# Kernel optimization log

Measured on AMD Instinct MI355X. Metric: run time of the kernel, lower is better.

## Reference

```python
import jax, jax.numpy as jnp
import numpy as np

N, M, DIST, HEADS, D, C, DFFN = 16384, 16, 2, 8, 256, 64, 512
DH = D // HEADS
GRID = 128
BLOCK = 2048  # mirrors torch batch_size loop in find_neighboring_voxels_optimized
EPS = 1e-5


def _neighbors(coords_f, src, m, dist):
    """Blockwise Manhattan-distance topk neighbor gather.
    coords_f: (N,3) float voxel coords; src: (N,D) features.
    Returns (N, m, D) neighbor features, zero-filled where fewer than m in range."""
    n = coords_f.shape[0]
    qblocks = coords_f.reshape(-1, BLOCK, 3)

    def one_block(cb):
        # (BLOCK, N) Manhattan distances
        d = jnp.abs(cb[:, None, :] - coords_f[None, :, :]).sum(-1)
        d = jnp.where(d <= dist, d, jnp.inf)
        vals, idx = jax.lax.top_k(-d, m)          # nearest m (self first: dist 0)
        valid = (vals > -jnp.inf)[..., None]
        return jnp.where(valid, src[idx], jnp.zeros((), src.dtype))

    return jax.lax.map(one_block, qblocks).reshape(n, m, src.shape[-1])


def _layernorm(x, g, b):
    mu = x.mean(-1, keepdims=True)
    var = ((x - mu) ** 2).mean(-1, keepdims=True)
    return (x - mu) * jax.lax.rsqrt(var + EPS) * g + b


def setup_inputs() -> dict:
    key = jax.random.key(0)
    ks = jax.random.split(key, 32)
    p = lambda i, shape, s: jax.random.normal(ks[i], shape, dtype=jnp.float32) * s
    z = lambda shape: jnp.zeros(shape, dtype=jnp.float32)
    o = lambda shape: jnp.ones(shape, dtype=jnp.float32)
    return {
        "coords": jax.random.randint(ks[0], (N, 3), 0, GRID, dtype=jnp.int32),
        "features": jax.random.normal(ks[1], (N, C), dtype=jnp.float32),
        "pe_w1": p(2, (3, D // 2), 0.5), "pe_b1": z((D // 2,)),
        "pe_w2": p(3, (D // 2, D), 0.08), "pe_b2": z((D,)),
        "proj_w": p(4, (C, D), 0.12), "proj_b": z((D,)),
        "wq": p(5, (D, D), 0.06), "bq": z((D,)),
        "wk": p(6, (D, D), 0.06), "bk": z((D,)),
        "wv": p(7, (D, D), 0.06), "bv": z((D,)),
        "wo": p(8, (D, D), 0.06), "bo": z((D,)),
        "ffn_w1": p(9, (D, DFFN), 0.06), "ffn_b1": z((DFFN,)),
        "ffn_w2": p(10, (DFFN, D), 0.04), "ffn_b2": z((D,)),
        "ln_g": o((D,)), "ln_b": z((D,)),
        "fus_w1": p(11, (D, C), 0.06), "fus_b1": z((C,)),
        "fus_w2": p(12, (2 * C, C), 0.09), "fus_b2": z((C,)),
        "bn_g": o((C,)), "bn_b": z((C,)),
    }


def reference(coords, features, pe_w1, pe_b1, pe_w2, pe_b2, proj_w, proj_b,
              wq, bq, wk, bk, wv, bv, wo, bo,
              ffn_w1, ffn_b1, ffn_w2, ffn_b2, ln_g, ln_b,
              fus_w1, fus_b1, fus_w2, fus_b2, bn_g, bn_b):
    coords_f = coords.astype(jnp.float32)
    # dynamic learnable positional encoding on normalized coords
    xn = coords_f / (GRID - 1)
    pe = jax.nn.relu(xn @ pe_w1 + pe_b1) @ pe_w2 + pe_b2
    src = features @ proj_w + proj_b + pe                       # (N, D)

    nf = _neighbors(coords_f, src, M, DIST)                     # (N, M, D)
    query = nf[:, 0, :]                                         # (N, D) self-feature

    # multihead attention: query len 1, key len M, batch N
    q = (query @ wq + bq).reshape(N, HEADS, DH)
    k = (nf @ wk + bk).reshape(N, M, HEADS, DH)
    v = (nf @ wv + bv).reshape(N, M, HEADS, DH)
    scores = jnp.einsum('nhd,nmhd->nhm', q, k) / jnp.sqrt(jnp.float32(DH))
    attn = jax.nn.softmax(scores, axis=-1)
    ao = jnp.einsum('nhm,nmhd->nhd', attn, v).reshape(N, D) @ wo + bo  # (N, D)

    # FFN with residual + LayerNorm (dropout=0 / eval)
    h = jax.nn.relu(ao @ ffn_w1 + ffn_b1) @ ffn_w2 + ffn_b2
    y = _layernorm(ao + h, ln_g, ln_b)                          # (N, D)

    # EnhancedFusion: project, concat, linear, BatchNorm1d (batch stats), ReLU
    t = y @ fus_w1 + fus_b1                                     # (N, C)
    f = jnp.concatenate([features, t], axis=1) @ fus_w2 + fus_b2
    mu = f.mean(0)
    var = ((f - mu) ** 2).mean(0)
    f = (f - mu) * jax.lax.rsqrt(var + EPS) * bn_g + bn_b
    return jax.nn.relu(f)                                       # (N, C)
```

## Files before the change

### kernel.cpp

```cpp
#include <hip/hip_runtime.h>
#include <stdint.h>

typedef unsigned short u16;
typedef unsigned int   u32;
typedef __attribute__((ext_vector_type(8))) short short8;
typedef __attribute__((ext_vector_type(4))) float f32x4;

static constexpr int kN = 16384;
static constexpr float kEPS = 1e-5f;

__device__ __forceinline__ u16 f2bf(float x) {
  u32 u = __float_as_uint(x);
  u32 r = (u + 0x7fffu + ((u >> 16) & 1u)) >> 16;
  return (u16)r;
}
__device__ __forceinline__ float bf2f(u16 x) {
  return __uint_as_float(((u32)x) << 16);
}
__device__ __forceinline__ void ldbf8(const u16* p, float* o) {
  uint4 v = *(const uint4*)p;
  o[0] = __uint_as_float(v.x << 16);  o[1] = __uint_as_float(v.x & 0xffff0000u);
  o[2] = __uint_as_float(v.y << 16);  o[3] = __uint_as_float(v.y & 0xffff0000u);
  o[4] = __uint_as_float(v.z << 16);  o[5] = __uint_as_float(v.z & 0xffff0000u);
  o[6] = __uint_as_float(v.w << 16);  o[7] = __uint_as_float(v.w & 0xffff0000u);
}


__global__ __launch_bounds__(256) void k_hist(const int* __restrict__ coords,
                                              u32* __restrict__ cnt) {
  int n = blockIdx.x * 256 + threadIdx.x;
  int c = coords[n * 3] * 128 + coords[n * 3 + 1];
  atomicAdd(&cnt[c], 1u);
}

__global__ __launch_bounds__(256) void k_scan(const u32* __restrict__ cnt,
                                              u32* __restrict__ startb) {
  __shared__ u32 tots[256];
  int t = threadIdx.x;
  int base = t * 64;
  u32 s = 0;
  for (int i = 0; i < 64; i++) s += cnt[base + i];
  tots[t] = s;
  __syncthreads();
  if (t == 0) {
    u32 run = 0;
    for (int i = 0; i < 256; i++) { u32 v = tots[i]; tots[i] = run; run += v; }
  }
  __syncthreads();
  u32 run = tots[t];
  for (int i = 0; i < 64; i++) { startb[base + i] = run; run += cnt[base + i]; }
}

__global__ __launch_bounds__(256) void k_scatter(const int* __restrict__ coords,
                                                 const u32* __restrict__ startb,
                                                 u32* __restrict__ cursor,
                                                 u32* __restrict__ pts) {
  int n = blockIdx.x * 256 + threadIdx.x;
  int x = coords[n * 3], y = coords[n * 3 + 1], z = coords[n * 3 + 2];
  int c = x * 128 + y;
  u32 slot = atomicAdd(&cursor[c], 1u);
  pts[startb[c] + slot] = ((u32)z << 14) | (u32)n;
}

__global__ __launch_bounds__(256) void k_select(const int* __restrict__ coords,
                                                const u32* __restrict__ startb,
                                                const u32* __restrict__ cnt,
                                                const u32* __restrict__ pts,
                                                int* __restrict__ idxo) {
  int n = blockIdx.x * 256 + threadIdx.x;
  int x = coords[n * 3], y = coords[n * 3 + 1], z = coords[n * 3 + 2];
  u32 best[16];
#pragma unroll
  for (int j = 0; j < 16; j++) best[j] = 0xFFFFFFFFu;
  const int dxs[13] = {0, -1, 1, 0, 0, -2, 2, 0, 0, -1, -1, 1, 1};
  const int dys[13] = {0, 0, 0, -1, 1, 0, 0, -2, 2, -1, 1, -1, 1};
  const int dbs[13] = {0, 1, 1, 1, 1, 2, 2, 2, 2, 2, 2, 2, 2};
#pragma unroll
  for (int t = 0; t < 13; t++) {
    int xx = x + dxs[t], yy = y + dys[t];
    if (xx < 0 || xx > 127 || yy < 0 || yy > 127) continue;
    int c = xx * 128 + yy;
    u32 s0 = startb[c], e0 = s0 + cnt[c];
    for (u32 i = s0; i < e0; ++i) {
      u32 p = pts[i];
      int zq = (int)(p >> 14);
      int id = (int)(p & 16383u);
      int az = z - zq; az = az < 0 ? -az : az;
      int dd = dbs[t] + az;
      u32 key = (dd <= 2) ? (((u32)dd << 14) | (u32)id) : 0xFFFFFFFFu;
#pragma unroll
      for (int j = 0; j < 16; j++) {
        u32 lo = min(best[j], key);
        u32 hi = max(best[j], key);
        best[j] = lo; key = hi;
      }
    }
  }
#pragma unroll
  for (int j = 0; j < 16; j++)
    idxo[n * 16 + j] = (best[j] == 0xFFFFFFFFu) ? -1 : (int)(best[j] & 16383u);
}

struct WSet {
  const float* s[8]; u16* d[8];
  int K[8]; int N[8]; int dstride[8]; int coff[8];
};

__global__ __launch_bounds__(256) void k_setup(WSet ws,
                                               u32* __restrict__ zero_area,
                                               const float* __restrict__ proj_b,
                                               const float* __restrict__ pe_b2,
                                               float* __restrict__ pbc,
                                               const float* __restrict__ uw1,
                                               const float* __restrict__ ub1,
                                               const float* __restrict__ uw2,
                                               const float* __restrict__ ub2,
                                               u16* __restrict__ W2f,
                                               float* __restrict__ bbf) {
  int w = blockIdx.y;
  if (w == 8) {
    zero_area[blockIdx.x * 256 + threadIdx.x] = 0u;
    return;
  }
  if (w == 9) {
    int bx = blockIdx.x;
    if (bx == 0) {
      pbc[threadIdx.x] = proj_b[threadIdx.x] + pe_b2[threadIdx.x];
    } else if (bx < 65) {
      int n = bx - 1;
      int k = threadIdx.x;
      float s = 0.f;
      for (int j = 0; j < 64; j++) s += uw1[k * 64 + j] * uw2[(64 + j) * 64 + n];
      W2f[n * 320 + k] = f2bf(s);
      if (k < 64) W2f[n * 320 + 256 + k] = f2bf(uw2[k * 64 + n]);
      if (k == 0) {
        float b = ub2[n];
        for (int j = 0; j < 64; j++) b += ub1[j] * uw2[(64 + j) * 64 + n];
        bbf[n] = b;
      }
    }
    return;
  }
  const float* S = ws.s[w]; u16* D = ws.d[w];
  int K = ws.K[w], N = ws.N[w], ds = ws.dstride[w], co = ws.coff[w];
  int ntx = N >> 5, tiles = ntx * (K >> 5);
  int t = blockIdx.x;
  if (t >= tiles) return;
  int n0 = (t % ntx) * 32, k0 = (t / ntx) * 32;
  __shared__ float st[32][33];
  int tr = threadIdx.x >> 3, tc4 = (threadIdx.x & 7) * 4;
  float4 v = *(const float4*)(S + (size_t)(k0 + tr) * N + n0 + tc4);
  st[tc4 + 0][tr] = v.x; st[tc4 + 1][tr] = v.y;
  st[tc4 + 2][tr] = v.z; st[tc4 + 3][tr] = v.w;
  __syncthreads();
  u16 o4[4];
  o4[0] = f2bf(st[tr][tc4 + 0]); o4[1] = f2bf(st[tr][tc4 + 1]);
  o4[2] = f2bf(st[tr][tc4 + 2]); o4[3] = f2bf(st[tr][tc4 + 3]);
  *(uint2*)(D + (size_t)(n0 + tr) * ds + co + k0 + tc4) = *(uint2*)o4;
}

__global__ __launch_bounds__(256) void k_prep(const int* __restrict__ coords,
                                              const float* __restrict__ feats,
                                              const float* __restrict__ pw1,
                                              const float* __restrict__ pb1,
                                              u16* __restrict__ A1,
                                              u16* __restrict__ A2) {
  int r0 = blockIdx.x * 32;
#pragma unroll
  for (int s = 0; s < 3; s++) {
    int j = threadIdx.x + s * 256;
    int row = j / 24, seg = j % 24;
    int n = r0 + row;
    u16 o[8];
    if (seg < 8) {
      const float* fp = feats + (size_t)n * 64 + seg * 8;
      float4 a = *(const float4*)fp;
      float4 b = *(const float4*)(fp + 4);
      o[0] = f2bf(a.x); o[1] = f2bf(a.y); o[2] = f2bf(a.z); o[3] = f2bf(a.w);
      o[4] = f2bf(b.x); o[5] = f2bf(b.y); o[6] = f2bf(b.z); o[7] = f2bf(b.w);
      *(uint4*)(A2 + (size_t)n * 320 + 256 + seg * 8) = *(uint4*)o;
    } else {
      int jj0 = (seg - 8) * 8;
      float x0 = (float)coords[n * 3 + 0] * (1.f / 127.f);
      float x1 = (float)coords[n * 3 + 1] * (1.f / 127.f);
      float x2 = (float)coords[n * 3 + 2] * (1.f / 127.f);
#pragma unroll
      for (int u = 0; u < 8; u++) {
        int jj = jj0 + u;
        float hv = pb1[jj] + x0 * pw1[jj] + x1 * pw1[128 + jj] + x2 * pw1[256 + jj];
        o[u] = f2bf(fmaxf(hv, 0.f));
      }
    }
    *(uint4*)(A1 + (size_t)n * 192 + seg * 8) = *(uint4*)o;
  }
}

template <int BM, int BN, int ACT, int OUTBF, int ADD>
__global__ __launch_bounds__(256) void k_mfma_gemm(
    const u16* __restrict__ A, const u16* __restrict__ WT,
    const float* __restrict__ bias,
    void* __restrict__ Cout,
    const u16* __restrict__ Addp,
    int M, int K, int N) {
  constexpr int GA = BM / 64;
  constexpr int GT = (BM + BN) / 64;
  constexpr int AI = BM / 32;
  constexpr int BI = BN / 32;
  __shared__ __align__(16) u16 As[BM * 32];
  __shared__ __align__(16) u16 Bs[BN * 32];
  const int tid = threadIdx.x;
  const int wave = tid >> 6, lane = tid & 63;
  const int bm = blockIdx.y * BM, bn = blockIdx.x * BN;
  const int wr = (wave >> 1) * (BM / 2), wc = (wave & 1) * (BN / 2);

  f32x4 acc[AI][BI];
#pragma unroll
  for (int i = 0; i < AI; i++)
#pragma unroll
    for (int j = 0; j < BI; j++)
#pragma unroll
      for (int r = 0; r < 4; r++) acc[i][j][r] = 0.f;

  for (int k0 = 0; k0 < K; k0 += 32) {
#pragma unroll
    for (int i = 0; i < GT; i++) {
      int g = i * 256 + wave * 64 + lane;
      if (i < GA) {
        int row = g >> 2, ko = (g & 3) * 8;
        __builtin_amdgcn_global_load_lds(
            (const __attribute__((address_space(1))) void*)(A + (size_t)(bm + row) * K + k0 + ko),
            (__attribute__((address_space(3))) void*)(As + (size_t)g * 8), 16, 0, 0);
      } else {
        int g2 = g - GA * 256;
        int row = g2 >> 2, ko = (g2 & 3) * 8;
        __builtin_amdgcn_global_load_lds(
            (const __attribute__((address_space(1))) void*)(WT + (size_t)(bn + row) * K + k0 + ko),
            (__attribute__((address_space(3))) void*)(Bs + (size_t)g2 * 8), 16, 0, 0);
      }
    }
    __syncthreads();
    short8 af[AI], bg[BI];
#pragma unroll
    for (int i = 0; i < AI; i++)
      af[i] = *(const short8*)&As[(wr + i * 16 + (lane & 15)) * 32 + (lane >> 4) * 8];
#pragma unroll
    for (int j = 0; j < BI; j++)
      bg[j] = *(const short8*)&Bs[(wc + j * 16 + (lane & 15)) * 32 + (lane >> 4) * 8];
#pragma unroll
    for (int i = 0; i < AI; i++)
#pragma unroll
      for (int j = 0; j < BI; j++)
        acc[i][j] = __builtin_amdgcn_mfma_f32_16x16x32_bf16(af[i], bg[j], acc[i][j], 0, 0, 0);
    __syncthreads();
  }

#pragma unroll
  for (int j = 0; j < BI; j++) {
    int cc = bn + wc + j * 16 + (lane & 15);
    float bval = bias ? bias[cc] : 0.f;
#pragma unroll
    for (int i = 0; i < AI; i++) {
      int rbase = bm + wr + i * 16 + (lane >> 4) * 4;
#pragma unroll
      for (int r = 0; r < 4; r++) {
        float v = acc[i][j][r] + bval;
        size_t o = (size_t)(rbase + r) * N + cc;
        if (ADD) v += bf2f(Addp[o]);
        if (ACT) v = fmaxf(v, 0.f);
        if (OUTBF) ((u16*)Cout)[o] = f2bf(v);
        else       ((float*)Cout)[o] = v;
      }
    }
  }
}

__global__ __launch_bounds__(256) void k_attn(const u16* __restrict__ QKV,
                                              const u32* __restrict__ pts,
                                              const int* __restrict__ idx,
                                              const float* __restrict__ bq,
                                              const float* __restrict__ bk,
                                              const float* __restrict__ bv,
                                              u16* __restrict__ outp) {
  int gid = blockIdx.x * 256 + threadIdx.x;
  int n = (int)(pts[gid >> 3] & 16383u), h = gid & 7;
  const int* ip = idx + n * 16;
  const int hb = h * 32;
  float q[32];
  {
    int i0 = ip[0];
    const u16* qp = QKV + (size_t)i0 * 768 + hb;
#pragma unroll
    for (int j = 0; j < 32; j += 8) ldbf8(qp + j, &q[j]);
#pragma unroll
    for (int j = 0; j < 32; j++) q[j] += bq[hb + j];
  }
// ... 26 lines not shown
#pragma unroll
  for (int j = 0; j < 32; j++) o[j] = 0.f;
#pragma unroll
  for (int m = 0; m < 16; m++) {
    if (ii[m] >= 0) {
      const u16* vp = QKV + (size_t)ii[m] * 768 + 512 + hb;
      float vv[32];
#pragma unroll
      for (int j = 0; j < 32; j += 8) ldbf8(vp + j, &vv[j]);
#pragma unroll
      for (int j = 0; j < 32; j++) o[j] += s[m] * vv[j];
    }
  }
  u16* op = outp + (size_t)n * 256 + hb;
#pragma unroll
  for (int j = 0; j < 32; j += 8) {
    u16 tmp[8];
#pragma unroll
    for (int jj = 0; jj < 8; jj++) tmp[jj] = f2bf(o[j + jj] * inv + bv[hb + j + jj]);
    *(uint4*)(op + j) = *(uint4*)tmp;
  }
}

__global__ __launch_bounds__(256) void k_ln(const u16* __restrict__ xx,
                                            const float* __restrict__ g,
                                            const float* __restrict__ b,
                                            u16* __restrict__ A2) {
  int row = blockIdx.x * 4 + (threadIdx.x >> 6);
  int lane = threadIdx.x & 63;
  uint2 raw = *(const uint2*)(xx + (size_t)row * 256 + lane * 4);
  float x0 = __uint_as_float(raw.x << 16), x1 = __uint_as_float(raw.x & 0xffff0000u);
  float x2 = __uint_as_float(raw.y << 16), x3 = __uint_as_float(raw.y & 0xffff0000u);
  float sm = x0 + x1 + x2 + x3;
#pragma unroll
  for (int off = 1; off < 64; off <<= 1) sm += __shfl_xor(sm, off);
  float mu = sm * (1.f / 256.f);
  float d0 = x0 - mu, d1 = x1 - mu, d2 = x2 - mu, d3 = x3 - mu;
  float sq = d0 * d0 + d1 * d1 + d2 * d2 + d3 * d3;
#pragma unroll
  for (int off = 1; off < 64; off <<= 1) sq += __shfl_xor(sq, off);
  float rstd = rsqrtf(sq * (1.f / 256.f) + kEPS);
  float4 gv = *(const float4*)(g + lane * 4);
  float4 bv4 = *(const float4*)(b + lane * 4);
  u16 o[4];
  o[0] = f2bf(d0 * rstd * gv.x + bv4.x); o[1] = f2bf(d1 * rstd * gv.y + bv4.y);
  o[2] = f2bf(d2 * rstd * gv.z + bv4.z); o[3] = f2bf(d3 * rstd * gv.w + bv4.w);
  *(uint2*)(A2 + (size_t)row * 320 + lane * 4) = *(uint2*)o;
}

__global__ __launch_bounds__(256) void k_stats(const float* __restrict__ f,
                                               float* __restrict__ pS, float* __restrict__ pQ) {
  int col = threadIdx.x & 63, rc = threadIdx.x >> 6;
  int r0 = blockIdx.x * 128 + rc * 32;
  float s = 0.f, q = 0.f;
  for (int r = 0; r < 32; r++) {
    float v = f[(size_t)(r0 + r) * 64 + col];
    s += v; q += v * v;
  }
  __shared__ float ls[4][64], lq[4][64];
  ls[rc][col] = s; lq[rc][col] = q;
  __syncthreads();
  if (rc == 0) {
    s = ls[0][col] + ls[1][col] + ls[2][col] + ls[3][col];
    q = lq[0][col] + lq[1][col] + lq[2][col] + lq[3][col];
    pS[blockIdx.x * 64 + col] = s;
    pQ[blockIdx.x * 64 + col] = q;
  }
}

__global__ __launch_bounds__(64) void k_bnfin(const float* __restrict__ pS,
                                              const float* __restrict__ pQ,
                                              const float* __restrict__ g,
                                              const float* __restrict__ b,
                                              float* __restrict__ coef,
                                              float* __restrict__ shift) {
  int c = threadIdx.x;
  float s = 0.f, q = 0.f;
  for (int i = 0; i < 128; i++) { s += pS[i * 64 + c]; q += pQ[i * 64 + c]; }
  float mu = s * (1.f / 16384.f);
  float var = q * (1.f / 16384.f) - mu * mu;
  float cf = rsqrtf(var + kEPS) * g[c];
  coef[c] = cf;
  shift[c] = b[c] - mu * cf;
}

__global__ __launch_bounds__(256) void k_bnapply(const float* __restrict__ f,
                                                 const float* __restrict__ coef,
                                                 const float* __restrict__ shift,
                                                 float* __restrict__ out) {
  int gid = blockIdx.x * 256 + threadIdx.x;
  int e = gid * 4, col = e & 63;
  float4 v = *(const float4*)(f + e);
  float4 cf = *(const float4*)(coef + col);
  float4 sh = *(const float4*)(shift + col);
  float4 o;
  o.x = fmaxf(v.x * cf.x + sh.x, 0.f);
  o.y = fmaxf(v.y * cf.y + sh.y, 0.f);
  o.z = fmaxf(v.z * cf.z + sh.z, 0.f);
  o.w = fmaxf(v.w * cf.w + sh.w, 0.f);
  *(float4*)(out + e) = o;
}

extern "C" void kernel_launch(void* const* d_in, const int* in_sizes, int n_in,
                              void* d_out, int out_size, void* d_ws, size_t ws_size,
                              hipStream_t stream) {
  (void)in_sizes; (void)n_in; (void)out_size; (void)ws_size;
// ... 10 lines not shown
  const float* wk  = (const float*)d_in[10];
  const float* bk  = (const float*)d_in[11];
  const float* wv  = (const float*)d_in[12];
  const float* bv  = (const float*)d_in[13];
  const float* wo  = (const float*)d_in[14];
  const float* bo  = (const float*)d_in[15];
  const float* fw1 = (const float*)d_in[16];
  const float* fb1 = (const float*)d_in[17];
  const float* fw2 = (const float*)d_in[18];
  const float* fb2 = (const float*)d_in[19];
  const float* lng = (const float*)d_in[20];
  const float* lnb = (const float*)d_in[21];
  const float* uw1 = (const float*)d_in[22];
  const float* ub1 = (const float*)d_in[23];
  const float* uw2 = (const float*)d_in[24];
  const float* ub2 = (const float*)d_in[25];
  const float* bng = (const float*)d_in[26];
  const float* bnb = (const float*)d_in[27];
  float* out = (float*)d_out;

  char* Wc = (char*)d_ws;
  const size_t MB = 1u << 20;
  u16*   A1    = (u16*)(Wc + 0 * MB);
  u16*   srcb  = (u16*)(Wc + 6 * MB);
  u16*   QKVb  = (u16*)(Wc + 14 * MB);
  u16*   aoInB = (u16*)(Wc + 38 * MB);
  u16*   aoB   = (u16*)(Wc + 46 * MB);
  u16*   h1B   = (u16*)(Wc + 54 * MB);
  u16*   xBb   = (u16*)(Wc + 70 * MB);
  u16*   A2    = (u16*)(Wc + 78 * MB);
  float* fB    = (float*)(Wc + 0 * MB);

  u16* qkvT  = (u16*)(Wc + 96 * MB);
  u16* woT   = qkvT + 196608;
  u16* fw1T  = woT + 65536;
  u16* fw2T  = fw1T + 131072;
  u16* W1T   = fw2T + 131072;
  u16* W2f   = W1T + 49152;
  float* pbc = (float*)(W2f + 20480);
  float* bbf = pbc + 256;

  u32* cnt    = (u32*)(Wc + 98 * MB);
  u32* cursor = cnt + 16384;
  u32* startb = cnt + 32768;
  u32* pts    = cnt + 49152;
  int* idxb   = (int*)(cnt + 65536);
  float* pS    = (float*)(cnt + 65536 + 262144);
  float* pQ    = pS + 8192;
  float* coefb = pQ + 8192;
  float* shb   = coefb + 64;

  WSet ws;
  ws.s[0] = wq;     ws.d[0] = qkvT;          ws.K[0] = 256; ws.N[0] = 256; ws.dstride[0] = 256; ws.coff[0] = 0;
  ws.s[1] = wk;     ws.d[1] = qkvT + 65536;  ws.K[1] = 256; ws.N[1] = 256; ws.dstride[1] = 256; ws.coff[1] = 0;
  ws.s[2] = wv;     ws.d[2] = qkvT + 131072; ws.K[2] = 256; ws.N[2] = 256; ws.dstride[2] = 256; ws.coff[2] = 0;
  ws.s[3] = wo;     ws.d[3] = woT;           ws.K[3] = 256; ws.N[3] = 256; ws.dstride[3] = 256; ws.coff[3] = 0;
  ws.s[4] = fw1;    ws.d[4] = fw1T;          ws.K[4] = 256; ws.N[4] = 512; ws.dstride[4] = 256; ws.coff[4] = 0;
  ws.s[5] = fw2;    ws.d[5] = fw2T;          ws.K[5] = 512; ws.N[5] = 256; ws.dstride[5] = 512; ws.coff[5] = 0;
  ws.s[6] = proj_w; ws.d[6] = W1T;           ws.K[6] = 64;  ws.N[6] = 256; ws.dstride[6] = 192; ws.coff[6] = 0;
  ws.s[7] = pe_w2;  ws.d[7] = W1T;           ws.K[7] = 128; ws.N[7] = 256; ws.dstride[7] = 192; ws.coff[7] = 64;
  k_setup<<<dim3(128, 10), 256, 0, stream>>>(ws, cnt, proj_b, pe_b2, pbc,
                                             uw1, ub1, uw2, ub2, W2f, bbf);

  k_hist<<<64, 256, 0, stream>>>(coords, cnt);
  k_scan<<<1, 256, 0, stream>>>(cnt, startb);
  k_scatter<<<64, 256, 0, stream>>>(coords, startb, cursor, pts);
  k_select<<<64, 256, 0, stream>>>(coords, startb, cnt, pts, idxb);

  k_prep<<<512, 256, 0, stream>>>(coords, feats, pe_w1, pe_b1, A1, A2);

  k_mfma_gemm<64, 64, 0, 1, 0><<<dim3(4, 256), 256, 0, stream>>>(A1, W1T, pbc, srcb, nullptr, kN, 192, 256);
  k_mfma_gemm<64, 64, 0, 1, 0><<<dim3(12, 256), 256, 0, stream>>>(srcb, qkvT, nullptr, QKVb, nullptr, kN, 256, 768);

  k_attn<<<512, 256, 0, stream>>>(QKVb, pts, idxb, bq, bk, bv, aoInB);

  k_mfma_gemm<64, 64, 0, 1, 0><<<dim3(4, 256), 256, 0, stream>>>(aoInB, woT, bo, aoB, nullptr, kN, 256, 256);
  k_mfma_gemm<64, 64, 1, 1, 0><<<dim3(8, 256), 256, 0, stream>>>(aoB, fw1T, fb1, h1B, nullptr, kN, 256, 512);
  k_mfma_gemm<64, 64, 0, 1, 1><<<dim3(4, 256), 256, 0, stream>>>(h1B, fw2T, fb2, xBb, aoB, kN, 512, 256);

  k_ln<<<4096, 256, 0, stream>>>(xBb, lng, lnb, A2);

  k_mfma_gemm<64, 64, 0, 0, 0><<<dim3(1, 256), 256, 0, stream>>>(A2, W2f, bbf, fB, nullptr, kN, 320, 64);

  k_stats<<<128, 256, 0, stream>>>(fB, pS, pQ);
  k_bnfin<<<1, 64, 0, stream>>>(pS, pQ, bng, bnb, coefb, shb);
  k_bnapply<<<1024, 256, 0, stream>>>(fB, coefb, shb, out);
}
```

Baseline: 257.6 us.

## Fuse pipeline into few kernels with grid barriers and on-chip intermediates

```diff
diff --git a/kernel.cpp b/kernel.cpp
--- a/kernel.cpp
+++ b/kernel.cpp
@@ -24,81 +24,10 @@
   o[4] = __uint_as_float(v.z << 16);  o[5] = __uint_as_float(v.z & 0xffff0000u);
   o[6] = __uint_as_float(v.w << 16);  o[7] = __uint_as_float(v.w & 0xffff0000u);
 }
-
-
-__global__ __launch_bounds__(256) void k_hist(const int* __restrict__ coords,
-                                              u32* __restrict__ cnt) {
-  int n = blockIdx.x * 256 + threadIdx.x;
-  int c = coords[n * 3] * 128 + coords[n * 3 + 1];
-  atomicAdd(&cnt[c], 1u);
-}
-
-__global__ __launch_bounds__(256) void k_scan(const u32* __restrict__ cnt,
-                                              u32* __restrict__ startb) {
-  __shared__ u32 tots[256];
-  int t = threadIdx.x;
-  int base = t * 64;
-  u32 s = 0;
-  for (int i = 0; i < 64; i++) s += cnt[base + i];
-  tots[t] = s;
-  __syncthreads();
-  if (t == 0) {
-    u32 run = 0;
-    for (int i = 0; i < 256; i++) { u32 v = tots[i]; tots[i] = run; run += v; }
-  }
-  __syncthreads();
-  u32 run = tots[t];
-  for (int i = 0; i < 64; i++) { startb[base + i] = run; run += cnt[base + i]; }
-}
-
-__global__ __launch_bounds__(256) void k_scatter(const int* __restrict__ coords,
-                                                 const u32* __restrict__ startb,
-                                                 u32* __restrict__ cursor,
-                                                 u32* __restrict__ pts) {
-  int n = blockIdx.x * 256 + threadIdx.x;
-  int x = coords[n * 3], y = coords[n * 3 + 1], z = coords[n * 3 + 2];
-  int c = x * 128 + y;
-  u32 slot = atomicAdd(&cursor[c], 1u);
-  pts[startb[c] + slot] = ((u32)z << 14) | (u32)n;
-}
-
-__global__ __launch_bounds__(256) void k_select(const int* __restrict__ coords,
-                                                const u32* __restrict__ startb,
-                                                const u32* __restrict__ cnt,
-                                                const u32* __restrict__ pts,
-                                                int* __restrict__ idxo) {
-  int n = blockIdx.x * 256 + threadIdx.x;
-  int x = coords[n * 3], y = coords[n * 3 + 1], z = coords[n * 3 + 2];
-  u32 best[16];
-#pragma unroll
-  for (int j = 0; j < 16; j++) best[j] = 0xFFFFFFFFu;
-  const int dxs[13] = {0, -1, 1, 0, 0, -2, 2, 0, 0, -1, -1, 1, 1};
-  const int dys[13] = {0, 0, 0, -1, 1, 0, 0, -2, 2, -1, 1, -1, 1};
-  const int dbs[13] = {0, 1, 1, 1, 1, 2, 2, 2, 2, 2, 2, 2, 2};
-#pragma unroll
-  for (int t = 0; t < 13; t++) {
-    int xx = x + dxs[t], yy = y + dys[t];
-    if (xx < 0 || xx > 127 || yy < 0 || yy > 127) continue;
-    int c = xx * 128 + yy;
-    u32 s0 = startb[c], e0 = s0 + cnt[c];
-    for (u32 i = s0; i < e0; ++i) {
-      u32 p = pts[i];
-      int zq = (int)(p >> 14);
-      int id = (int)(p & 16383u);
-      int az = z - zq; az = az < 0 ? -az : az;
-      int dd = dbs[t] + az;
-      u32 key = (dd <= 2) ? (((u32)dd << 14) | (u32)id) : 0xFFFFFFFFu;
-#pragma unroll
-      for (int j = 0; j < 16; j++) {
-        u32 lo = min(best[j], key);
-        u32 hi = max(best[j], key);
-        best[j] = lo; key = hi;
-      }
-    }
-  }
-#pragma unroll
-  for (int j = 0; j < 16; j++)
-    idxo[n * 16 + j] = (best[j] == 0xFFFFFFFFu) ? -1 : (int)(best[j] & 16383u);
+__device__ __forceinline__ void gll16(const u16* g, u16* l) {
+  __builtin_amdgcn_global_load_lds(
+      (const __attribute__((address_space(1))) void*)g,
+      (__attribute__((address_space(3))) void*)l, 16, 0, 0);
 }
 
 struct WSet {
@@ -116,10 +45,17 @@
                                                const float* __restrict__ uw2,
                                                const float* __restrict__ ub2,
                                                u16* __restrict__ W2f,
-                                               float* __restrict__ bbf) {
+                                               float* __restrict__ bbf,
+                                               const int* __restrict__ coords,
+                                               const float* __restrict__ feats,
+                                               const float* __restrict__ pw1,
+                                               const float* __restrict__ pb1,
+                                               u16* __restrict__ A1,
+                                               u16* __restrict__ A2) {
   int w = blockIdx.y;
   if (w == 8) {
-    zero_area[blockIdx.x * 256 + threadIdx.x] = 0u;
+    int idx = blockIdx.x * 256 + threadIdx.x;
+    if (idx < 32960) zero_area[idx] = 0u;
     return;
   }
   if (w == 9) {
@@ -141,6 +77,39 @@
     }
     return;
   }
+  if (w == 10) {
+    int r0 = blockIdx.x * 32;
+#pragma unroll
+    for (int s = 0; s < 3; s++) {
+      int j = threadIdx.x + s * 256;
+      int row = j / 24, seg = j % 24;
+      int n = r0 + row;
+      u16 o[8];
+      if (seg < 8) {
+        const float* fp = feats + (size_t)n * 64 + seg * 8;
+        float4 a = *(const float4*)fp;
+        float4 b = *(const float4*)(fp + 4);
+        o[0] = f2bf(a.x); o[1] = f2bf(a.y); o[2] = f2bf(a.z); o[3] = f2bf(a.w);
+        o[4] = f2bf(b.x); o[5] = f2bf(b.y); o[6] = f2bf(b.z); o[7] = f2bf(b.w);
+        *(uint4*)(A2 + (size_t)n * 320 + 256 + seg * 8) = *(uint4*)o;
+      } else {
+        int jj0 = (seg - 8) * 8;
+        float x0 = (float)coords[n * 3 + 0] * (1.f / 127.f);
+        float x1 = (float)coords[n * 3 + 1] * (1.f / 127.f);
+        float x2 = (float)coords[n * 3 + 2] * (1.f / 127.f);
+#pragma unroll
+        for (int u = 0; u < 8; u++) {
+          int jj = jj0 + u;
+          float hv = pb1[jj] + x0 * pw1[jj] + x1 * pw1[128 + jj] + x2 * pw1[256 + jj];
+          o[u] = f2bf(fmaxf(hv, 0.f));
+        }
+        *(uint4*)(A1 + (size_t)n * 192 + seg * 8) = *(uint4*)o;
+        continue;
+      }
+      *(uint4*)(A1 + (size_t)n * 192 + seg * 8) = *(uint4*)o;
+    }
+    return;
+  }
   const float* S = ws.s[w]; u16* D = ws.d[w];
   int K = ws.K[w], N = ws.N[w], ds = ws.dstride[w], co = ws.coff[w];
   int ntx = N >> 5, tiles = ntx * (K >> 5);
@@ -159,118 +128,195 @@
   *(uint2*)(D + (size_t)(n0 + tr) * ds + co + k0 + tc4) = *(uint2*)o4;
 }
 
-__global__ __launch_bounds__(256) void k_prep(const int* __restrict__ coords,
-                                              const float* __restrict__ feats,
-                                              const float* __restrict__ pw1,
-                                              const float* __restrict__ pb1,
-                                              u16* __restrict__ A1,
-                                              u16* __restrict__ A2) {
-  int r0 = blockIdx.x * 32;
-#pragma unroll
-  for (int s = 0; s < 3; s++) {
-    int j = threadIdx.x + s * 256;
-    int row = j / 24, seg = j % 24;
-    int n = r0 + row;
-    u16 o[8];
-    if (seg < 8) {
-      const float* fp = feats + (size_t)n * 64 + seg * 8;
-      float4 a = *(const float4*)fp;
-      float4 b = *(const float4*)(fp + 4);
-      o[0] = f2bf(a.x); o[1] = f2bf(a.y); o[2] = f2bf(a.z); o[3] = f2bf(a.w);
-      o[4] = f2bf(b.x); o[5] = f2bf(b.y); o[6] = f2bf(b.z); o[7] = f2bf(b.w);
-      *(uint4*)(A2 + (size_t)n * 320 + 256 + seg * 8) = *(uint4*)o;
-    } else {
-      int jj0 = (seg - 8) * 8;
-      float x0 = (float)coords[n * 3 + 0] * (1.f / 127.f);
-      float x1 = (float)coords[n * 3 + 1] * (1.f / 127.f);
-      float x2 = (float)coords[n * 3 + 2] * (1.f / 127.f);
-#pragma unroll
-      for (int u = 0; u < 8; u++) {
-        int jj = jj0 + u;
-        float hv = pb1[jj] + x0 * pw1[jj] + x1 * pw1[128 + jj] + x2 * pw1[256 + jj];
-        o[u] = f2bf(fmaxf(hv, 0.f));
-      }
-    }
-    *(uint4*)(A1 + (size_t)n * 192 + seg * 8) = *(uint4*)o;
-  }
-}
-
-template <int BM, int BN, int ACT, int OUTBF, int ADD>
-__global__ __launch_bounds__(256) void k_mfma_gemm(
-    const u16* __restrict__ A, const u16* __restrict__ WT,
-    const float* __restrict__ bias,
-    void* __restrict__ Cout,
-    const u16* __restrict__ Addp,
-    int M, int K, int N) {
-  constexpr int GA = BM / 64;
-  constexpr int GT = (BM + BN) / 64;
-  constexpr int AI = BM / 32;
-  constexpr int BI = BN / 32;
-  __shared__ __align__(16) u16 As[BM * 32];
-  __shared__ __align__(16) u16 Bs[BN * 32];
+__device__ __forceinline__ void gbar(u32* bar, u32 target) {
+  __syncthreads();
+  if (threadIdx.x == 0) {
+    __threadfence();
+    __hip_atomic_fetch_add(bar, 1u, __ATOMIC_RELEASE, __HIP_MEMORY_SCOPE_AGENT);
+    while (__hip_atomic_load(bar, __ATOMIC_ACQUIRE, __HIP_MEMORY_SCOPE_AGENT) < target) {}
+    __threadfence();
+  }
+  __syncthreads();
+}
+
+__global__ __launch_bounds__(256) void k_grid(const int* __restrict__ coords,
+                                              u32* __restrict__ cnt,
+                                              u32* __restrict__ cursor,
+                                              u32* __restrict__ startb,
+                                              u32* __restrict__ pts,
+                                              int* __restrict__ idxo,
+                                              u32* __restrict__ bar) {
+  int n = blockIdx.x * 256 + threadIdx.x;
+  int x = coords[n * 3], y = coords[n * 3 + 1], z = coords[n * 3 + 2];
+  int c = x * 128 + y;
+  atomicAdd(&cnt[c], 1u);
+  gbar(bar, 64);
+  if (blockIdx.x == 0) {
+    __shared__ u32 tots[256];
+    int t = threadIdx.x;
+    int base = t * 64;
+    u32 s = 0;
+    for (int i = 0; i < 64; i++) s += cnt[base + i];
+    tots[t] = s;
+    __syncthreads();
+    if (t == 0) {
+      u32 run = 0;
+      for (int i = 0; i < 256; i++) { u32 v = tots[i]; tots[i] = run; run += v; }
+    }
+    __syncthreads();
+    u32 run = tots[t];
+    for (int i = 0; i < 64; i++) { startb[base + i] = run; run += cnt[base + i]; }
+  }
+  gbar(bar, 128);
+  {
+    u32 slot = atomicAdd(&cursor[c], 1u);
+    pts[startb[c] + slot] = ((u32)z << 14) | (u32)n;
+  }
+  gbar(bar, 192);
+  {
+    u32 best[16];
+#pragma unroll
+    for (int j = 0; j < 16; j++) best[j] = 0xFFFFFFFFu;
+    const int dxs[13] = {0, -1, 1, 0, 0, -2, 2, 0, 0, -1, -1, 1, 1};
+    const int dys[13] = {0, 0, 0, -1, 1, 0, 0, -2, 2, -1, 1, -1, 1};
+    const int dbs[13] = {0, 1, 1, 1, 1, 2, 2, 2, 2, 2, 2, 2, 2};
+#pragma unroll
+    for (int t = 0; t < 13; t++) {
+      int xx = x + dxs[t], yy = y + dys[t];
+      if (xx < 0 || xx > 127 || yy < 0 || yy > 127) continue;
+      int cc = xx * 128 + yy;
+      u32 s0 = startb[cc], e0 = s0 + cnt[cc];
+      for (u32 i = s0; i < e0; ++i) {
+        u32 p = pts[i];
+        int zq = (int)(p >> 14);
+        int id = (int)(p & 16383u);
+        int az = z - zq; az = az < 0 ? -az : az;
+        int dd = dbs[t] + az;
+        u32 key = (dd <= 2) ? (((u32)dd << 14) | (u32)id) : 0xFFFFFFFFu;
+#pragma unroll
+        for (int j = 0; j < 16; j++) {
+          u32 lo = min(best[j], key);
+          u32 hi = max(best[j], key);
+          best[j] = lo; key = hi;
+        }
+      }
+    }
+#pragma unroll
+    for (int j = 0; j < 16; j++)
+      idxo[n * 16 + j] = (best[j] == 0xFFFFFFFFu) ? -1 : (int)(best[j] & 16383u);
+  }
+}
+
+__global__ __launch_bounds__(256) void k_src_qkv(const u16* __restrict__ A1,
+                                                 const u16* __restrict__ W1T,
+                                                 const float* __restrict__ pbc,
+                                                 const u16* __restrict__ qkvT,
+                                                 u16* __restrict__ QKV) {
+  __shared__ __align__(16) u16 reg1[16896];
+  __shared__ __align__(16) u16 srcL[16896];
+  __shared__ __align__(16) u16 Bs[2048];
   const int tid = threadIdx.x;
   const int wave = tid >> 6, lane = tid & 63;
-  const int bm = blockIdx.y * BM, bn = blockIdx.x * BN;
-  const int wr = (wave >> 1) * (BM / 2), wc = (wave & 1) * (BN / 2);
-
-  f32x4 acc[AI][BI];
-#pragma unroll
-  for (int i = 0; i < AI; i++)
-#pragma unroll
-    for (int j = 0; j < BI; j++)
-#pragma unroll
-      for (int r = 0; r < 4; r++) acc[i][j][r] = 0.f;
-
-  for (int k0 = 0; k0 < K; k0 += 32) {
-#pragma unroll
-    for (int i = 0; i < GT; i++) {
-      int g = i * 256 + wave * 64 + lane;
-      if (i < GA) {
+  const int bm = blockIdx.x * 64;
+  const int wr = (wave >> 1) * 32, wc = (wave & 1) * 32;
+  const int fr = lane & 15, fk = (lane >> 4) * 8, rq = (lane >> 4) * 4;
+
+#pragma unroll
+  for (int s = 0; s < 6; s++) {
+    int c = tid + s * 256;
+    int row = c / 24, kc = c % 24;
+    *(uint4*)&reg1[row * 200 + kc * 8] =
+        *(const uint4*)(A1 + (size_t)(bm + row) * 192 + kc * 8);
+  }
+  __syncthreads();
+
+  for (int nc = 0; nc < 4; nc++) {
+    f32x4 acc[2][2];
+#pragma unroll
+    for (int i = 0; i < 2; i++)
+#pragma unroll
+      for (int j = 0; j < 2; j++)
+#pragma unroll
+        for (int r = 0; r < 4; r++) acc[i][j][r] = 0.f;
+    for (int k0 = 0; k0 < 192; k0 += 32) {
+      {
+        int g = wave * 64 + lane;
         int row = g >> 2, ko = (g & 3) * 8;
-        __builtin_amdgcn_global_load_lds(
-            (const __attribute__((address_space(1))) void*)(A + (size_t)(bm + row) * K + k0 + ko),
-            (__attribute__((address_space(3))) void*)(As + (size_t)g * 8), 16, 0, 0);
-      } else {
-        int g2 = g - GA * 256;
-        int row = g2 >> 2, ko = (g2 & 3) * 8;
-        __builtin_amdgcn_global_load_lds(
-            (const __attribute__((address_space(1))) void*)(WT + (size_t)(bn + row) * K + k0 + ko),
-            (__attribute__((address_space(3))) void*)(Bs + (size_t)g2 * 8), 16, 0, 0);
-      }
+        gll16(W1T + (size_t)(nc * 64 + row) * 192 + k0 + ko, Bs + g * 8);
+      }
+      __syncthreads();
+      short8 af[2], bg[2];
+#pragma unroll
+      for (int i = 0; i < 2; i++)
+        af[i] = *(const short8*)&reg1[(wr + i * 16 + fr) * 200 + k0 + fk];
+#pragma unroll
+      for (int j = 0; j < 2; j++)
+        bg[j] = *(const short8*)&Bs[(wc + j * 16 + fr) * 32 + fk];
+#pragma unroll
+      for (int i = 0; i < 2; i++)
+#pragma unroll
+        for (int j = 0; j < 2; j++)
+          acc[i][j] = __builtin_amdgcn_mfma_f32_16x16x32_bf16(af[i], bg[j], acc[i][j], 0, 0, 0);
+      __syncthreads();
+    }
+#pragma unroll
+    for (int j = 0; j < 2; j++) {
+      int col = nc * 64 + wc + j * 16 + fr;
+      float bv = pbc[col];
+#pragma unroll
+      for (int i = 0; i < 2; i++) {
+        int rb = wr + i * 16 + rq;
+#pragma unroll
+        for (int r = 0; r < 4; r++)
+          srcL[(rb + r) * 264 + col] = f2bf(acc[i][j][r] + bv);
+      }
+    }
+  }
+  __syncthreads();
+
+  for (int qc = 0; qc < 12; qc++) {
+#pragma unroll
+    for (int s = 0; s < 8; s++) {
+      int c = tid + s * 256;
+      int row = c >> 5, kc = c & 31;
+      *(uint4*)&reg1[row * 264 + kc * 8] =
+          *(const uint4*)(qkvT + (size_t)(qc * 64 + row) * 256 + kc * 8);
     }
     __syncthreads();
-    short8 af[AI], bg[BI];
-#pragma unroll
-    for (int i = 0; i < AI; i++)
-      af[i] = *(const short8*)&As[(wr + i * 16 + (lane & 15)) * 32 + (lane >> 4) * 8];
-#pragma unroll
-    for (int j = 0; j < BI; j++)
-      bg[j] = *(const short8*)&Bs[(wc + j * 16 + (lane & 15)) * 32 + (lane >> 4) * 8];
-#pragma unroll
-    for (int i = 0; i < AI; i++)
-#pragma unroll
-      for (int j = 0; j < BI; j++)
-        acc[i][j] = __builtin_amdgcn_mfma_f32_16x16x32_bf16(af[i], bg[j], acc[i][j], 0, 0, 0);
+    f32x4 acc[2][2];
+#pragma unroll
+    for (int i = 0; i < 2; i++)
+#pragma unroll
+      for (int j = 0; j < 2; j++)
+#pragma unroll
+        for (int r = 0; r < 4; r++) acc[i][j][r] = 0.f;
+#pragma unroll
+    for (int k0 = 0; k0 < 256; k0 += 32) {
+      short8 af[2], bg[2];
+#pragma unroll
+      for (int i = 0; i < 2; i++)
+        af[i] = *(const short8*)&srcL[(wr + i * 16 + fr) * 264 + k0 + fk];
+#pragma unroll
+      for (int j = 0; j < 2; j++)
+        bg[j] = *(const short8*)&reg1[(wc + j * 16 + fr) * 264 + k0 + fk];
+#pragma unroll
+      for (int i = 0; i < 2; i++)
+#pragma unroll
+        for (int j = 0; j < 2; j++)
+          acc[i][j] = __builtin_amdgcn_mfma_f32_16x16x32_bf16(af[i], bg[j], acc[i][j], 0, 0, 0);
+    }
+#pragma unroll
+    for (int j = 0; j < 2; j++) {
+      int col = qc * 64 + wc + j * 16 + fr;
+#pragma unroll
+      for (int i = 0; i < 2; i++) {
+        int rb = wr + i * 16 + rq;
+#pragma unroll
+        for (int r = 0; r < 4; r++)
+          QKV[(size_t)(bm + rb + r) * 768 + col] = f2bf(acc[i][j][r]);
+      }
+    }
     __syncthreads();
-  }
-
-#pragma unroll
-  for (int j = 0; j < BI; j++) {
-    int cc = bn + wc + j * 16 + (lane & 15);
-    float bval = bias ? bias[cc] : 0.f;
-#pragma unroll
-    for (int i = 0; i < AI; i++) {
-      int rbase = bm + wr + i * 16 + (lane >> 4) * 4;
-#pragma unroll
-      for (int r = 0; r < 4; r++) {
-        float v = acc[i][j][r] + bval;
-        size_t o = (size_t)(rbase + r) * N + cc;
-        if (ADD) v += bf2f(Addp[o]);
-        if (ACT) v = fmaxf(v, 0.f);
-        if (OUTBF) ((u16*)Cout)[o] = f2bf(v);
-        else       ((float*)Cout)[o] = v;
-      }
-    }
   }
 }
 
@@ -343,66 +389,315 @@
   }
 }
 
-__global__ __launch_bounds__(256) void k_ln(const u16* __restrict__ xx,
-                                            const float* __restrict__ g,
-                                            const float* __restrict__ b,
-                                            u16* __restrict__ A2) {
-  int row = blockIdx.x * 4 + (threadIdx.x >> 6);
-  int lane = threadIdx.x & 63;
-  uint2 raw = *(const uint2*)(xx + (size_t)row * 256 + lane * 4);
-  float x0 = __uint_as_float(raw.x << 16), x1 = __uint_as_float(raw.x & 0xffff0000u);
-  float x2 = __uint_as_float(raw.y << 16), x3 = __uint_as_float(raw.y & 0xffff0000u);
-  float sm = x0 + x1 + x2 + x3;
-#pragma unroll
-  for (int off = 1; off < 64; off <<= 1) sm += __shfl_xor(sm, off);
-  float mu = sm * (1.f / 256.f);
-  float d0 = x0 - mu, d1 = x1 - mu, d2 = x2 - mu, d3 = x3 - mu;
-  float sq = d0 * d0 + d1 * d1 + d2 * d2 + d3 * d3;
-#pragma unroll
-  for (int off = 1; off < 64; off <<= 1) sq += __shfl_xor(sq, off);
-  float rstd = rsqrtf(sq * (1.f / 256.f) + kEPS);
-  float4 gv = *(const float4*)(g + lane * 4);
-  float4 bv4 = *(const float4*)(b + lane * 4);
-  u16 o[4];
-  o[0] = f2bf(d0 * rstd * gv.x + bv4.x); o[1] = f2bf(d1 * rstd * gv.y + bv4.y);
-  o[2] = f2bf(d2 * rstd * gv.z + bv4.z); o[3] = f2bf(d3 * rstd * gv.w + bv4.w);
-  *(uint2*)(A2 + (size_t)row * 320 + lane * 4) = *(uint2*)o;
-}
-
-__global__ __launch_bounds__(256) void k_stats(const float* __restrict__ f,
-                                               float* __restrict__ pS, float* __restrict__ pQ) {
-  int col = threadIdx.x & 63, rc = threadIdx.x >> 6;
-  int r0 = blockIdx.x * 128 + rc * 32;
-  float s = 0.f, q = 0.f;
-  for (int r = 0; r < 32; r++) {
-    float v = f[(size_t)(r0 + r) * 64 + col];
-    s += v; q += v * v;
-  }
-  __shared__ float ls[4][64], lq[4][64];
-  ls[rc][col] = s; lq[rc][col] = q;
-  __syncthreads();
-  if (rc == 0) {
-    s = ls[0][col] + ls[1][col] + ls[2][col] + ls[3][col];
-    q = lq[0][col] + lq[1][col] + lq[2][col] + lq[3][col];
-    pS[blockIdx.x * 64 + col] = s;
-    pQ[blockIdx.x * 64 + col] = q;
-  }
-}
-
-__global__ __launch_bounds__(64) void k_bnfin(const float* __restrict__ pS,
-                                              const float* __restrict__ pQ,
-                                              const float* __restrict__ g,
-                                              const float* __restrict__ b,
+__global__ __launch_bounds__(256) void k_ffn_ln(const u16* __restrict__ aoIn,
+                                                const u16* __restrict__ woT,
+                                                const float* __restrict__ bo,
+                                                const u16* __restrict__ fw1T,
+                                                const float* __restrict__ fb1,
+                                                const u16* __restrict__ fw2T,
+                                                const float* __restrict__ fb2,
+                                                const float* __restrict__ lng,
+                                                const float* __restrict__ lnb,
+                                                u16* __restrict__ A2) {
+  __shared__ __align__(16) u16 aoL[16896];
+  __shared__ __align__(16) u16 h1L[16896];
+  __shared__ __align__(16) u16 As[2048];
+  __shared__ __align__(16) u16 Bs[2048];
+  const int tid = threadIdx.x;
+  const int wave = tid >> 6, lane = tid & 63;
+  const int bm = blockIdx.x * 64;
+  const int wr = (wave >> 1) * 32, wc = (wave & 1) * 32;
+  const int fr = lane & 15, fk = (lane >> 4) * 8, rq = (lane >> 4) * 4;
+  const int g = wave * 64 + lane;
+  const int grow = g >> 2, gko = (g & 3) * 8;
+
+  for (int nc = 0; nc < 4; nc++) {
+    f32x4 acc[2][2];
+#pragma unroll
+    for (int i = 0; i < 2; i++)
+#pragma unroll
+      for (int j = 0; j < 2; j++)
+#pragma unroll
+        for (int r = 0; r < 4; r++) acc[i][j][r] = 0.f;
+    for (int k0 = 0; k0 < 256; k0 += 32) {
+      gll16(aoIn + (size_t)(bm + grow) * 256 + k0 + gko, As + g * 8);
+      gll16(woT + (size_t)(nc * 64 + grow) * 256 + k0 + gko, Bs + g * 8);
+      __syncthreads();
+      short8 af[2], bg[2];
+#pragma unroll
+      for (int i = 0; i < 2; i++)
+        af[i] = *(const short8*)&As[(wr + i * 16 + fr) * 32 + fk];
+#pragma unroll
+      for (int j = 0; j < 2; j++)
+        bg[j] = *(const short8*)&Bs[(wc + j * 16 + fr) * 32 + fk];
+#pragma unroll
+      for (int i = 0; i < 2; i++)
+#pragma unroll
+        for (int j = 0; j < 2; j++)
+          acc[i][j] = __builtin_amdgcn_mfma_f32_16x16x32_bf16(af[i], bg[j], acc[i][j], 0, 0, 0);
+      __syncthreads();
+    }
+#pragma unroll
+    for (int j = 0; j < 2; j++) {
+      int col = nc * 64 + wc + j * 16 + fr;
+      float bv = bo[col];
+#pragma unroll
+      for (int i = 0; i < 2; i++) {
+        int rb = wr + i * 16 + rq;
+#pragma unroll
+        for (int r = 0; r < 4; r++)
+          aoL[(rb + r) * 264 + col] = f2bf(acc[i][j][r] + bv);
+      }
+    }
+  }
+  __syncthreads();
+
+  f32x4 xacc[4][2][2];
+#pragma unroll
+  for (int xc = 0; xc < 4; xc++)
+#pragma unroll
+    for (int i = 0; i < 2; i++)
+#pragma unroll
+      for (int j = 0; j < 2; j++)
+#pragma unroll
+        for (int r = 0; r < 4; r++) xacc[xc][i][j][r] = 0.f;
+
+  for (int h = 0; h < 2; h++) {
+    for (int nc = 0; nc < 4; nc++) {
+      f32x4 acc[2][2];
+#pragma unroll
+      for (int i = 0; i < 2; i++)
+#pragma unroll
+        for (int j = 0; j < 2; j++)
+#pragma unroll
+          for (int r = 0; r < 4; r++) acc[i][j][r] = 0.f;
+      for (int k0 = 0; k0 < 256; k0 += 32) {
+        gll16(fw1T + (size_t)(h * 256 + nc * 64 + grow) * 256 + k0 + gko, Bs + g * 8);
+        __syncthreads();
+        short8 af[2], bg[2];
+#pragma unroll
+        for (int i = 0; i < 2; i++)
+          af[i] = *(const short8*)&aoL[(wr + i * 16 + fr) * 264 + k0 + fk];
+#pragma unroll
+        for (int j = 0; j < 2; j++)
+          bg[j] = *(const short8*)&Bs[(wc + j * 16 + fr) * 32 + fk];
+#pragma unroll
+        for (int i = 0; i < 2; i++)
+#pragma unroll
+          for (int j = 0; j < 2; j++)
+            acc[i][j] = __builtin_amdgcn_mfma_f32_16x16x32_bf16(af[i], bg[j], acc[i][j], 0, 0, 0);
+        __syncthreads();
+      }
+#pragma unroll
+      for (int j = 0; j < 2; j++) {
+        int col = nc * 64 + wc + j * 16 + fr;
+        float bv = fb1[h * 256 + col];
+#pragma unroll
+        for (int i = 0; i < 2; i++) {
+          int rb = wr + i * 16 + rq;
+#pragma unroll
+          for (int r = 0; r < 4; r++)
+            h1L[(rb + r) * 264 + col] = f2bf(fmaxf(acc[i][j][r] + bv, 0.f));
+        }
+      }
+    }
+    __syncthreads();
+    for (int xc = 0; xc < 4; xc++) {
+      for (int k0 = 0; k0 < 256; k0 += 32) {
+        gll16(fw2T + (size_t)(xc * 64 + grow) * 512 + h * 256 + k0 + gko, Bs + g * 8);
+        __syncthreads();
+        short8 af[2], bg[2];
+#pragma unroll
+        for (int i = 0; i < 2; i++)
+          af[i] = *(const short8*)&h1L[(wr + i * 16 + fr) * 264 + k0 + fk];
+#pragma unroll
+        for (int j = 0; j < 2; j++)
+          bg[j] = *(const short8*)&Bs[(wc + j * 16 + fr) * 32 + fk];
+#pragma unroll
+        for (int i = 0; i < 2; i++)
+#pragma unroll
+          for (int j = 0; j < 2; j++)
+            xacc[xc][i][j] = __builtin_amdgcn_mfma_f32_16x16x32_bf16(af[i], bg[j], xacc[xc][i][j], 0, 0, 0);
+        __syncthreads();
+      }
+    }
+  }
+
+  float rowS[2][4], rowQ[2][4];
+#pragma unroll
+  for (int i = 0; i < 2; i++)
+#pragma unroll
+    for (int r = 0; r < 4; r++) { rowS[i][r] = 0.f; rowQ[i][r] = 0.f; }
+#pragma unroll
+  for (int xc = 0; xc < 4; xc++)
+#pragma unroll
+    for (int j = 0; j < 2; j++) {
+      int col = xc * 64 + wc + j * 16 + fr;
+      float f2 = fb2[col];
+#pragma unroll
+      for (int i = 0; i < 2; i++) {
+        int rb = wr + i * 16 + rq;
+#pragma unroll
+        for (int r = 0; r < 4; r++) {
+          float v = xacc[xc][i][j][r] + f2 + bf2f(aoL[(rb + r) * 264 + col]);
+          xacc[xc][i][j][r] = v;
+          rowS[i][r] += v; rowQ[i][r] += v * v;
+        }
+      }
+    }
+#pragma unroll
+  for (int off = 1; off < 16; off <<= 1) {
+#pragma unroll
+    for (int i = 0; i < 2; i++)
+#pragma unroll
+      for (int r = 0; r < 4; r++) {
+        rowS[i][r] += __shfl_xor(rowS[i][r], off);
+        rowQ[i][r] += __shfl_xor(rowQ[i][r], off);
+      }
+  }
+  float* redS = (float*)As;
+  float* redQ = redS + 128;
+  if (fr == 0) {
+#pragma unroll
+    for (int i = 0; i < 2; i++)
+#pragma unroll
+      for (int r = 0; r < 4; r++) {
+        int row = wr + i * 16 + rq + r;
+        redS[row * 2 + (wave & 1)] = rowS[i][r];
+        redQ[row * 2 + (wave & 1)] = rowQ[i][r];
+      }
+  }
+  __syncthreads();
+  float mu[2][4], rs[2][4];
+#pragma unroll
+  for (int i = 0; i < 2; i++)
+#pragma unroll
+    for (int r = 0; r < 4; r++) {
+      int row = wr + i * 16 + rq + r;
+      float S = redS[row * 2] + redS[row * 2 + 1];
+      float Q = redQ[row * 2] + redQ[row * 2 + 1];
+      float m = S * (1.f / 256.f);
+      mu[i][r] = m;
+      rs[i][r] = rsqrtf(Q * (1.f / 256.f) - m * m + kEPS);
+    }
+#pragma unroll
+  for (int xc = 0; xc < 4; xc++)
+#pragma unroll
+    for (int j = 0; j < 2; j++) {
+      int col = xc * 64 + wc + j * 16 + fr;
+      float g_ = lng[col], b_ = lnb[col];
+#pragma unroll
+      for (int i = 0; i < 2; i++) {
+        int rb = wr + i * 16 + rq;
+#pragma unroll
+        for (int r = 0; r < 4; r++) {
+          float yv = (xacc[xc][i][j][r] - mu[i][r]) * rs[i][r] * g_ + b_;
+          A2[(size_t)(bm + rb + r) * 320 + col] = f2bf(yv);
+        }
+      }
+    }
+}
+
+__global__ __launch_bounds__(256) void k_tail(const u16* __restrict__ A2,
+                                              const u16* __restrict__ W2f,
+                                              const float* __restrict__ bbf,
+                                              float* __restrict__ fB,
+                                              float* __restrict__ pS,
+                                              float* __restrict__ pQ,
+                                              u32* __restrict__ arrive,
+                                              const float* __restrict__ bng,
+                                              const float* __restrict__ bnb,
                                               float* __restrict__ coef,
                                               float* __restrict__ shift) {
-  int c = threadIdx.x;
-  float s = 0.f, q = 0.f;
-  for (int i = 0; i < 128; i++) { s += pS[i * 64 + c]; q += pQ[i * 64 + c]; }
-  float mu = s * (1.f / 16384.f);
-  float var = q * (1.f / 16384.f) - mu * mu;
-  float cf = rsqrtf(var + kEPS) * g[c];
-  coef[c] = cf;
-  shift[c] = b[c] - mu * cf;
+  __shared__ __align__(16) u16 As[2048];
+  __shared__ __align__(16) u16 Bs[2048];
+  __shared__ float colS[64][2], colQ[64][2];
+  __shared__ u32 lastf;
+  const int tid = threadIdx.x;
+  const int wave = tid >> 6, lane = tid & 63;
+  const int bm = blockIdx.x * 64;
+  const int wr = (wave >> 1) * 32, wc = (wave & 1) * 32;
+  const int fr = lane & 15, fk = (lane >> 4) * 8, rq = (lane >> 4) * 4;
+  const int g = wave * 64 + lane;
+  const int grow = g >> 2, gko = (g & 3) * 8;
+
+  f32x4 acc[2][2];
+#pragma unroll
+  for (int i = 0; i < 2; i++)
+#pragma unroll
+    for (int j = 0; j < 2; j++)
+#pragma unroll
+      for (int r = 0; r < 4; r++) acc[i][j][r] = 0.f;
+  for (int k0 = 0; k0 < 320; k0 += 32) {
+    gll16(A2 + (size_t)(bm + grow) * 320 + k0 + gko, As + g * 8);
+    gll16(W2f + (size_t)grow * 320 + k0 + gko, Bs + g * 8);
+    __syncthreads();
+    short8 af[2], bg[2];
+#pragma unroll
+    for (int i = 0; i < 2; i++)
+      af[i] = *(const short8*)&As[(wr + i * 16 + fr) * 32 + fk];
+#pragma unroll
+    for (int j = 0; j < 2; j++)
+      bg[j] = *(const short8*)&Bs[(wc + j * 16 + fr) * 32 + fk];
+#pragma unroll
+    for (int i = 0; i < 2; i++)
+#pragma unroll
+      for (int j = 0; j < 2; j++)
+        acc[i][j] = __builtin_amdgcn_mfma_f32_16x16x32_bf16(af[i], bg[j], acc[i][j], 0, 0, 0);
+    __syncthreads();
+  }
+  float cS[2] = {0.f, 0.f}, cQ[2] = {0.f, 0.f};
+#pragma unroll
+  for (int j = 0; j < 2; j++) {
+    int col = wc + j * 16 + fr;
+    float bv = bbf[col];
+#pragma unroll
+    for (int i = 0; i < 2; i++) {
+      int rb = wr + i * 16 + rq;
+#pragma unroll
+      for (int r = 0; r < 4; r++) {
+        float v = acc[i][j][r] + bv;
+        fB[(size_t)(bm + rb + r) * 64 + col] = v;
+        cS[j] += v; cQ[j] += v * v;
+      }
+    }
+  }
+#pragma unroll
+  for (int off = 16; off < 64; off <<= 1) {
+#pragma unroll
+    for (int j = 0; j < 2; j++) {
+      cS[j] += __shfl_xor(cS[j], off);
+      cQ[j] += __shfl_xor(cQ[j], off);
+    }
+  }
+  if ((lane >> 4) == 0) {
+#pragma unroll
+    for (int j = 0; j < 2; j++) {
+      colS[wc + j * 16 + fr][wave >> 1] = cS[j];
+      colQ[wc + j * 16 + fr][wave >> 1] = cQ[j];
+    }
+  }
+  __syncthreads();
+  if (tid < 64) {
+    atomicAdd(&pS[tid], colS[tid][0] + colS[tid][1]);
+    atomicAdd(&pQ[tid], colQ[tid][0] + colQ[tid][1]);
+  }
+  __syncthreads();
+  if (tid == 0) {
+    __threadfence();
+    u32 old = __hip_atomic_fetch_add(arrive, 1u, __ATOMIC_ACQ_REL, __HIP_MEMORY_SCOPE_AGENT);
+    lastf = (old == 255) ? 1u : 0u;
+  }
+  __syncthreads();
+  if (lastf && tid < 64) {
+    float S = __hip_atomic_load(&pS[tid], __ATOMIC_ACQUIRE, __HIP_MEMORY_SCOPE_AGENT);
+    float Q = __hip_atomic_load(&pQ[tid], __ATOMIC_ACQUIRE, __HIP_MEMORY_SCOPE_AGENT);
+    float m = S * (1.f / 16384.f);
+    float var = Q * (1.f / 16384.f) - m * m;
+    float cf = rsqrtf(var + kEPS) * bng[tid];
+    coef[tid] = cf;
+    shift[tid] = bnb[tid] - m * cf;
+  }
 }
 
 __global__ __launch_bounds__(256) void k_bnapply(const float* __restrict__ f,
@@ -459,16 +754,12 @@
   char* Wc = (char*)d_ws;
   const size_t MB = 1u << 20;
   u16*   A1    = (u16*)(Wc + 0 * MB);
-  u16*   srcb  = (u16*)(Wc + 6 * MB);
-  u16*   QKVb  = (u16*)(Wc + 14 * MB);
-  u16*   aoInB = (u16*)(Wc + 38 * MB);
-  u16*   aoB   = (u16*)(Wc + 46 * MB);
-  u16*   h1B   = (u16*)(Wc + 54 * MB);
-  u16*   xBb   = (u16*)(Wc + 70 * MB);
-  u16*   A2    = (u16*)(Wc + 78 * MB);
-  float* fB    = (float*)(Wc + 0 * MB);
-
-  u16* qkvT  = (u16*)(Wc + 96 * MB);
+  u16*   QKVb  = (u16*)(Wc + 6 * MB);
+  u16*   aoInB = (u16*)(Wc + 30 * MB);
+  u16*   A2    = (u16*)(Wc + 38 * MB);
+  float* fB    = (float*)(Wc + 48 * MB);
+
+  u16* qkvT  = (u16*)(Wc + 52 * MB);
   u16* woT   = qkvT + 196608;
   u16* fw1T  = woT + 65536;
   u16* fw2T  = fw1T + 131072;
@@ -477,15 +768,18 @@
   float* pbc = (float*)(W2f + 20480);
   float* bbf = pbc + 256;
 
-  u32* cnt    = (u32*)(Wc + 98 * MB);
-  u32* cursor = cnt + 16384;
-  u32* startb = cnt + 32768;
-  u32* pts    = cnt + 49152;
-  int* idxb   = (int*)(cnt + 65536);
-  float* pS    = (float*)(cnt + 65536 + 262144);
-  float* pQ    = pS + 8192;
-  float* coefb = pQ + 8192;
+  u32* Z      = (u32*)(Wc + 56 * MB);
+  u32* cnt    = Z;
+  u32* cursor = Z + 16384;
+  float* pS   = (float*)(Z + 32768);
+  float* pQ   = (float*)(Z + 32832);
+  u32* bar    = Z + 32896;
+  u32* arrive = Z + 32897;
+  float* coefb = (float*)(Z + 32912);
   float* shb   = coefb + 64;
+  u32* startb = Z + 33280;
+  u32* pts    = Z + 49664;
+  int* idxb   = (int*)(Z + 82432);
 
   WSet ws;
   ws.s[0] = wq;     ws.d[0] = qkvT;          ws.K[0] = 256; ws.N[0] = 256; ws.dstride[0] = 256; ws.coff[0] = 0;
@@ -496,30 +790,14 @@
   ws.s[5] = fw2;    ws.d[5] = fw2T;          ws.K[5] = 512; ws.N[5] = 256; ws.dstride[5] = 512; ws.coff[5] = 0;
   ws.s[6] = proj_w; ws.d[6] = W1T;           ws.K[6] = 64;  ws.N[6] = 256; ws.dstride[6] = 192; ws.coff[6] = 0;
   ws.s[7] = pe_w2;  ws.d[7] = W1T;           ws.K[7] = 128; ws.N[7] = 256; ws.dstride[7] = 192; ws.coff[7] = 64;
-  k_setup<<<dim3(128, 10), 256, 0, stream>>>(ws, cnt, proj_b, pe_b2, pbc,
-                                             uw1, ub1, uw2, ub2, W2f, bbf);
-
-  k_hist<<<64, 256, 0, stream>>>(coords, cnt);
-  k_scan<<<1, 256, 0, stream>>>(cnt, startb);
-  k_scatter<<<64, 256, 0, stream>>>(coords, startb, cursor, pts);
-  k_select<<<64, 256, 0, stream>>>(coords, startb, cnt, pts, idxb);
-
-  k_prep<<<512, 256, 0, stream>>>(coords, feats, pe_w1, pe_b1, A1, A2);
-
-  k_mfma_gemm<64, 64, 0, 1, 0><<<dim3(4, 256), 256, 0, stream>>>(A1, W1T, pbc, srcb, nullptr, kN, 192, 256);
-  k_mfma_gemm<64, 64, 0, 1, 0><<<dim3(12, 256), 256, 0, stream>>>(srcb, qkvT, nullptr, QKVb, nullptr, kN, 256, 768);
-
+
+  k_setup<<<dim3(512, 11), 256, 0, stream>>>(ws, Z, proj_b, pe_b2, pbc,
+                                             uw1, ub1, uw2, ub2, W2f, bbf,
+                                             coords, feats, pe_w1, pe_b1, A1, A2);
+  k_grid<<<64, 256, 0, stream>>>(coords, cnt, cursor, startb, pts, idxb, bar);
+  k_src_qkv<<<256, 256, 0, stream>>>(A1, W1T, pbc, qkvT, QKVb);
   k_attn<<<512, 256, 0, stream>>>(QKVb, pts, idxb, bq, bk, bv, aoInB);
-
-  k_mfma_gemm<64, 64, 0, 1, 0><<<dim3(4, 256), 256, 0, stream>>>(aoInB, woT, bo, aoB, nullptr, kN, 256, 256);
-  k_mfma_gemm<64, 64, 1, 1, 0><<<dim3(8, 256), 256, 0, stream>>>(aoB, fw1T, fb1, h1B, nullptr, kN, 256, 512);
-  k_mfma_gemm<64, 64, 0, 1, 1><<<dim3(4, 256), 256, 0, stream>>>(h1B, fw2T, fb2, xBb, aoB, kN, 512, 256);
-
-  k_ln<<<4096, 256, 0, stream>>>(xBb, lng, lnb, A2);
-
-  k_mfma_gemm<64, 64, 0, 0, 0><<<dim3(1, 256), 256, 0, stream>>>(A2, W2f, bbf, fB, nullptr, kN, 320, 64);
-
-  k_stats<<<128, 256, 0, stream>>>(fB, pS, pQ);
-  k_bnfin<<<1, 64, 0, stream>>>(pS, pQ, bng, bnb, coefb, shb);
+  k_ffn_ln<<<256, 256, 0, stream>>>(aoInB, woT, bo, fw1T, fb1, fw2T, fb2, lng, lnb, A2);
+  k_tail<<<256, 256, 0, stream>>>(A2, W2f, bbf, fB, pS, pQ, arrive, bng, bnb, coefb, shb);
   k_bnapply<<<1024, 256, 0, stream>>>(fB, coefb, shb, out);
 }
```

New measurement: 291.6 us. +13.2%, slower.
